# Kernel tuning notes

Measured on AMD Instinct MI355X. Metric: run time of the kernel, lower is better.

The kernel has to match this reference:

```python
import jax, jax.numpy as jnp
import numpy as np
import math

N_HEAD = 16
HEAD_QKV = 1024  # total qkv width; head_dim = HEAD_QKV // N_HEAD
WM_DECAY_LENGTH = 2048
WM_DECAY_RATE = 1.0
WM_ECHOIC = 16


def decay_weight_matrix(n):
    # power_law decay, faithful to get_decay_weight_matrix
    dl = WM_DECAY_LENGTH - WM_ECHOIC + 1
    nums = jnp.linspace(0.0, 1.0, dl)
    decay_values = 1.0 - jnp.power(nums, 1.0 / (np.e * WM_DECAY_RATE))
    decay_values = jnp.concatenate([jnp.ones(WM_ECHOIC - 1), decay_values])  # [WM_DECAY_LENGTH]
    decay_values = decay_values[:n]
    idx = jnp.arange(n)[:, None] - jnp.arange(n)[None, :]  # [n,n], negative above diag
    mat = decay_values[jnp.clip(idx, 0, n - 1)]
    return jnp.tril(mat).astype(jnp.float32)


def setup_inputs() -> dict:
    key = jax.random.key(0)
    k1, k2, k3 = jax.random.split(key, 3)
    B, T, C = 2, 2048, 1024
    x = jax.random.normal(k1, (B, T, C), dtype=jnp.float32)
    W_attn = jax.random.normal(k2, (C, 3 * HEAD_QKV), dtype=jnp.float32) * (1.0 / math.sqrt(C))
    W_proj = jax.random.normal(k3, (HEAD_QKV, C), dtype=jnp.float32) * (1.0 / math.sqrt(HEAD_QKV))
    return {"x": x, "W_attn": W_attn, "W_proj": W_proj}


def reference(x, W_attn, W_proj):
    B, T, C = x.shape
    hd = HEAD_QKV // N_HEAD
    qkv = x @ W_attn  # [B,T,3*HEAD_QKV]
    q, k, v = jnp.split(qkv, 3, axis=-1)
    # [B,T,HQKV] -> [B,H,T,hd]
    q = q.reshape(B, T, N_HEAD, hd).transpose(0, 2, 1, 3)
    k = k.reshape(B, T, N_HEAD, hd).transpose(0, 2, 1, 3)
    v = v.reshape(B, T, N_HEAD, hd).transpose(0, 2, 1, 3)
    att = jnp.einsum('bhqd,bhkd->bhqk', q, k) * (1.0 / math.sqrt(hd))
    causal = jnp.tril(jnp.ones((T, T), dtype=bool))
    att = jnp.where(causal, att, -jnp.inf)
    att = jax.nn.softmax(att, axis=-1)
    att = att * decay_weight_matrix(T)  # post-softmax multiplicative decay
    y = jnp.einsum('bhqk,bhkd->bhqd', att, v)
    y = y.transpose(0, 2, 1, 3).reshape(B, T, HEAD_QKV)
    return y @ W_proj
```

## Files before the change

kernel.cpp:

```cpp
#include <hip/hip_runtime.h>
#include <math.h>

#define B_  2
#define T_  2048
#define C_  1024
#define NH_ 16
#define HD_ 64
#define N3_ 3072

typedef float f32x4 __attribute__((ext_vector_type(4)));
typedef short bf16x8 __attribute__((ext_vector_type(8)));
typedef unsigned short u16;
typedef float f32x4_base __attribute__((ext_vector_type(4)));
typedef f32x4_base __attribute__((aligned(4))) f32x4u;

#define QSCALE 0.18033688011112042f

#if __has_builtin(__builtin_amdgcn_exp2f)
#define EXP2(x) __builtin_amdgcn_exp2f(x)
#else
#define EXP2(x) exp2f(x)
#endif

__device__ __forceinline__ u16 f2bf(float x) {
  unsigned int u = __builtin_bit_cast(unsigned int, x);
  u += 0x7FFFu + ((u >> 16) & 1u);
  return (u16)(u >> 16);
}

__device__ __forceinline__ unsigned int cvt_pk_bf16(float lo, float hi) {
  unsigned int r;
  asm("v_cvt_pk_bf16_f32 %0, %1, %2" : "=v"(r) : "v"(lo), "v"(hi));
  return r;
}

#define GLD16(g, l) __builtin_amdgcn_global_load_lds( \
    (__attribute__((address_space(1))) void*)(g), \
    (__attribute__((address_space(3))) void*)(l), 16, 0, 0)

__global__ __launch_bounds__(256) void prep_kernel(
    const float* __restrict__ x, u16* __restrict__ xb,
    const float* __restrict__ Wa, u16* __restrict__ WaT,
    const float* __restrict__ Wp, u16* __restrict__ WpT,
    float* __restrict__ decR)
{
  __shared__ float tile[32][33];
  const int bid = blockIdx.x;
  const int tid = threadIdx.x;
  if (bid < 4096) {
    int i = (bid * 256 + tid) * 4;
    float4 v = *(const float4*)(x + i);
    ushort4 o;
    o.x = f2bf(v.x); o.y = f2bf(v.y); o.z = f2bf(v.z); o.w = f2bf(v.w);
    *(ushort4*)(xb + i) = o;
  } else if (bid < 8192) {
    const float* in; u16* out; int Cc, c0, r0;
    if (bid < 7168) {
      int t = bid - 4096;
      in = Wa; out = WaT; Cc = N3_;
      c0 = (t % 96) * 32; r0 = (t / 96) * 32;
    } else {
      int t = bid - 7168;
      in = Wp; out = WpT; Cc = C_;
      c0 = (t % 32) * 32; r0 = (t / 32) * 32;
    }
    int tx = tid & 31, ty = tid >> 5;
#pragma unroll
    for (int rr = ty; rr < 32; rr += 8)
      tile[rr][tx] = in[(size_t)(r0 + rr) * Cc + c0 + tx];
    __syncthreads();
#pragma unroll
    for (int rr = ty; rr < 32; rr += 8)
      out[(size_t)(c0 + rr) * 1024 + r0 + tx] = f2bf(tile[tx][rr]);
  } else {
    int j = (bid - 8192) * 256 + tid;
    if (j < 4352) {
      int d = 2047 - j;
      float v = 1.0f;
      if (d >= 15) v = 1.0f - powf((float)(d - 15) * (1.0f / 2032.0f), 0.36787944117144233f);
      decR[j] = v;
    }
  }
}

template<int MODE>
__global__ __launch_bounds__(256, 3) void gemm128_kernel(
    const u16* __restrict__ A, const u16* __restrict__ Bt,
    float* __restrict__ Cf, u16* __restrict__ Cq, u16* __restrict__ Vt,
    int M, int N, int K)
{
  __shared__ char lds[49152];
  const int lane = threadIdx.x & 63;
  const int wave = threadIdx.x >> 6;
  const int nxb = N >> 7;
  const int orig = blockIdx.x;
  const int cpx = (int)gridDim.x >> 3;
  const int wg = (orig & 7) * cpx + (orig >> 3);
  const int m0 = (wg / nxb) << 7;
  const int n0 = (wg % nxb) << 7;
  const int wm = wave >> 1, wn = wave & 1;

  f32x4 acc[4][4] = {};

#define GSTAGE(buf, k0)                                                          \
  {                                                                              \
    _Pragma("unroll")                                                            \
    for (int c = 0; c < 2; ++c) {                                                \
      int chunk = wave * 2048 + c * 1024;                                        \
      int row = (chunk >> 6) + (lane >> 2);                                      \
      int wb = ((lane & 3) << 4) ^ ((row & 3) << 4);                             \
      GLD16((const char*)(A  + (size_t)(m0 + row) * K + (k0)) + wb,              \
            lds + (buf) * 16384 + chunk);                                        \
      GLD16((const char*)(Bt + (size_t)(n0 + row) * K + (k0)) + wb,              \
            lds + (buf) * 16384 + 8192 + chunk);                                 \
    }                                                                            \
  }

  const int nk = K >> 5;
  GSTAGE(0, 0);
  GSTAGE(1, 32);
  __syncthreads();

  for (int i = 0; i < nk; ++i) {
    if (i + 1 < nk) asm volatile("s_waitcnt vmcnt(4)" ::: "memory");
    else            asm volatile("s_waitcnt vmcnt(0)" ::: "memory");
    __builtin_amdgcn_s_barrier();
    __builtin_amdgcn_sched_barrier(0);
    if (i + 2 < nk) GSTAGE((i + 2) % 3, (i + 2) * 32);

    const char* base = lds + (i % 3) * 16384;
    bf16x8 af[4], bfr[4];
#pragma unroll
    for (int m = 0; m < 4; ++m) {
      int row = wm * 64 + m * 16 + (lane & 15);
      int wb = ((lane >> 4) << 4) ^ ((row & 3) << 4);
      af[m] = *(const bf16x8*)(base + row * 64 + wb);
    }
#pragma unroll
    for (int n = 0; n < 4; ++n) {
      int row = wn * 64 + n * 16 + (lane & 15);
      int wb = ((lane >> 4) << 4) ^ ((row & 3) << 4);
      bfr[n] = *(const bf16x8*)(base + 8192 + row * 64 + wb);
    }
    __builtin_amdgcn_s_setprio(1);
#pragma unroll
    for (int m = 0; m < 4; ++m)
#pragma unroll
      for (int n = 0; n < 4; ++n)
        acc[m][n] = __builtin_amdgcn_mfma_f32_16x16x32_bf16(af[m], bfr[n], acc[m][n], 0, 0, 0);
    __builtin_amdgcn_s_setprio(0);
  }

#pragma unroll
  for (int m = 0; m < 4; ++m) {
    int grow0 = m0 + wm * 64 + m * 16 + ((lane >> 4) << 2);
#pragma unroll
    for (int n = 0; n < 4; ++n) {
      int gcol = n0 + wn * 64 + n * 16 + (lane & 15);
      f32x4 v = acc[m][n];
      if (MODE == 0) {
        int bb = grow0 >> 11, tt0 = grow0 & 2047;
        int which = gcol >> 10, rem = gcol & 1023;
        int hh = rem >> 6, dd = rem & 63;
        if (which < 2) {
#pragma unroll
          for (int r = 0; r < 4; ++r) {
            float ov = (which == 0) ? v[r] * QSCALE : v[r];
            Cq[((size_t)(which * 32 + bb * 16 + hh) * 2048 + tt0 + r) * 64 + dd] = f2bf(ov);
          }
        } else {
          ushort4 o;
          o.x = f2bf(v[0]); o.y = f2bf(v[1]); o.z = f2bf(v[2]); o.w = f2bf(v[3]);
          *(ushort4*)(Vt + ((size_t)(bb * 16 + hh) * 64 + dd) * 2048 + tt0) = o;
        }
      } else {
#pragma unroll
        for (int r = 0; r < 4; ++r)
          Cf[(size_t)(grow0 + r) * N + gcol] = v[r];
      }
    }
  }
#undef GSTAGE
}

__global__ __launch_bounds__(256, 2) void attn_kernel(
    const u16* __restrict__ qkb, const u16* __restrict__ vtg,
    const float* __restrict__ decR, u16* __restrict__ yb)
{
  __shared__ char klds[2][8192];
  __shared__ char vlds[2][8192];
  __shared__ u16 plds[128 * 76];

  const int lane = threadIdx.x & 63;
  const int wave = threadIdx.x >> 6;
  const int quad = lane >> 4;
  const int l15 = lane & 15;
  const int orig = blockIdx.x;
  const int xcd = orig & 7;
  const int j = orig >> 3;
  const int bh = xcd * 4 + (j & 3);
  const int tt = j >> 2;
  const int qtA = (tt < 8) ? tt : 23 - tt;
  const int qtB = 31 - qtA;
  const int b = bh >> 4, h = bh & 15;

  const u16* Q   = qkb + (size_t)bh * T_ * HD_;
  const u16* Kg  = qkb + (size_t)(32 + bh) * T_ * HD_;
  const u16* VTg = vtg + (size_t)bh * HD_ * T_;

  const int wrowB = qtB * 64 + wave * 16;
  const int wrowA = qtA * 64 + wave * 16;
  const int qB = wrowB + l15;
  const int qA = wrowA + l15;
  const float* dpB = decR + (2047 - qB + quad * 4);
  const float* dpA = decR + (2047 - qA + quad * 4);

  bf16x8 qaB[2], qaA[2];
  { const u16* qp = Q + (size_t)qB * HD_ + quad * 8;
    qaB[0] = *(const bf16x8*)qp; qaB[1] = *(const bf16x8*)(qp + 32); }
  { const u16* qp = Q + (size_t)qA * HD_ + quad * 8;
    qaA[0] = *(const bf16x8*)qp; qaA[1] = *(const bf16x8*)(qp + 32); }

  f32x4 accB[4] = {}, accA[4] = {};
  float lsumB = 0.0f, lsumA = 0.0f;

#define ASTAGE(buf, kt)                                                          \
  {                                                                              \
    _Pragma("unroll")                                                            \
    for (int c = 0; c < 2; ++c) {                                                \
      int chunk = wave * 2048 + c * 1024;                                        \
      int row = (chunk >> 7) + (lane >> 3);                                      \
      int wb = ((lane & 7) << 4) ^ ((row & 7) << 4);                             \
      GLD16((const char*)(Kg + (size_t)((kt) * 64 + row) * HD_) + wb,            \
            klds[buf] + chunk);                                                  \
      GLD16((const char*)(VTg + (size_t)row * T_ + (kt) * 64) + wb,              \
            vlds[buf] + chunk);                                                  \
    }                                                                            \
  }

  f32x4 dBc[4], dAc[4], dBn[4], dAn[4];
#pragma unroll
  for (int f = 0; f < 4; ++f) {
    dBn[f] = *(const f32x4u*)(dpB + f * 16);
    dAn[f] = *(const f32x4u*)(dpA + f * 16);
  }
  ASTAGE(0, 0);
  __syncthreads();

  const int nkt = qtB + 1;
  for (int kt = 0; kt < nkt; ++kt) {
    const int cur = kt & 1;
#pragma unroll
    for (int f = 0; f < 4; ++f) { dBc[f] = dBn[f]; dAc[f] = dAn[f]; }
    const float* dB1 = dpB + (kt + 1) * 64;
    const float* dA1 = dpA + (kt + 1) * 64;
#pragma unroll
    for (int f = 0; f < 4; ++f) {
      dBn[f] = *(const f32x4u*)(dB1 + f * 16);
      dAn[f] = *(const f32x4u*)(dA1 + f * 16);
    }
    asm volatile("s_waitcnt vmcnt(8)" ::: "memory");
    __builtin_amdgcn_s_barrier();
    __builtin_amdgcn_sched_barrier(0);
    if (kt + 1 < nkt) ASTAGE(cur ^ 1, kt + 1);

    const bool actA = (kt <= qtA);

    bf16x8 kf[4][2];
#pragma unroll
    for (int f = 0; f < 4; ++f) {
      int krow = f * 16 + l15;
      int base = krow * 128;
      int msk = (krow & 7) << 4;
      kf[f][0] = *(const bf16x8*)(klds[cur] + base + ((quad * 16) ^ msk));
      kf[f][1] = *(const bf16x8*)(klds[cur] + base + ((64 + quad * 16) ^ msk));
    }

    f32x4 sB[4], sA[4];
    __builtin_amdgcn_s_setprio(1);
#pragma unroll
    for (int f = 0; f < 4; ++f) {
      f32x4 t = {};
      t = __builtin_amdgcn_mfma_f32_16x16x32_bf16(kf[f][0], qaB[0], t, 0, 0, 0);
      t = __builtin_amdgcn_mfma_f32_16x16x32_bf16(kf[f][1], qaB[1], t, 0, 0, 0);
      sB[f] = t;
    }
    if (actA) {
#pragma unroll
      for (int f = 0; f < 4; ++f) {
        f32x4 t = {};
        t = __builtin_amdgcn_mfma_f32_16x16x32_bf16(kf[f][0], qaA[0], t, 0, 0, 0);
        t = __builtin_amdgcn_mfma_f32_16x16x32_bf16(kf[f][1], qaA[1], t, 0, 0, 0);
        sA[f] = t;
      }
    }
    __builtin_amdgcn_s_setprio(0);

    if (kt == qtB) {
#pragma unroll
      for (int f = 0; f < 4; ++f) {
        int key0 = kt * 64 + f * 16 + quad * 4;
#pragma unroll
        for (int r = 0; r < 4; ++r)
          if (key0 + r > qB) sB[f][r] = -1e30f;
      }
    }
    if (actA && kt == qtA) {
#pragma unroll
      for (int f = 0; f < 4; ++f) {
        int key0 = kt * 64 + f * 16 + quad * 4;
#pragma unroll
        for (int r = 0; r < 4; ++r)
          if (key0 + r > qA) sA[f][r] = -1e30f;
      }
    }

#pragma unroll
    for (int f = 0; f < 4; ++f) {
      f32x4 p;
#pragma unroll
      for (int r = 0; r < 4; ++r) p[r] = EXP2(sB[f][r]);
      lsumB += (p[0] + p[1]) + (p[2] + p[3]);
      unsigned int w0 = cvt_pk_bf16(p[0] * dBc[f][0], p[1] * dBc[f][1]);
      unsigned int w1 = cvt_pk_bf16(p[2] * dBc[f][2], p[3] * dBc[f][3]);
      uint2 wv; wv.x = w0; wv.y = w1;
      *(uint2*)(plds + (size_t)(wave * 16 + l15) * 76 + f * 16 + quad * 4) = wv;
    }
    if (actA) {
#pragma unroll
      for (int f = 0; f < 4; ++f) {
        f32x4 p;
#pragma unroll
        for (int r = 0; r < 4; ++r) p[r] = EXP2(sA[f][r]);
        lsumA += (p[0] + p[1]) + (p[2] + p[3]);
        unsigned int w0 = cvt_pk_bf16(p[0] * dAc[f][0], p[1] * dAc[f][1]);
        unsigned int w1 = cvt_pk_bf16(p[2] * dAc[f][2], p[3] * dAc[f][3]);
        uint2 wv; wv.x = w0; wv.y = w1;
        *(uint2*)(plds + (size_t)(64 + wave * 16 + l15) * 76 + f * 16 + quad * 4) = wv;
      }
    }

    bf16x8 vf[4][2];
#pragma unroll
    for (int n = 0; n < 4; ++n) {
      int vrow = n * 16 + l15;
      int mskv = (vrow & 7) << 4;
#pragma unroll
      for (int ks = 0; ks < 2; ++ks)
        vf[n][ks] = *(const bf16x8*)(vlds[cur] + vrow * 128 + ((ks * 64 + quad * 16) ^ mskv));
    }

    __builtin_amdgcn_s_setprio(1);
#pragma unroll
    for (int ks = 0; ks < 2; ++ks) {
      bf16x8 pa = *(const bf16x8*)(plds + (size_t)(wave * 16 + l15) * 76 + ks * 32 + quad * 8);
#pragma unroll
      for (int n = 0; n < 4; ++n)
        accB[n] = __builtin_amdgcn_mfma_f32_16x16x32_bf16(pa, vf[n][ks], accB[n], 0, 0, 0);
    }
    if (actA) {
#pragma unroll
      for (int ks = 0; ks < 2; ++ks) {
        bf16x8 pa = *(const bf16x8*)(plds + (size_t)(64 + wave * 16 + l15) * 76 + ks * 32 + quad * 8);
#pragma unroll
        for (int n = 0; n < 4; ++n)
          accA[n] = __builtin_amdgcn_mfma_f32_16x16x32_bf16(pa, vf[n][ks], accA[n], 0, 0, 0);
      }
    }
    __builtin_amdgcn_s_setprio(0);
  }
#undef ASTAGE

  lsumB += __shfl_xor(lsumB, 16); lsumB += __shfl_xor(lsumB, 32);
  lsumA += __shfl_xor(lsumA, 16); lsumA += __shfl_xor(lsumA, 32);
  float rB[4], rA[4];
#pragma unroll
  for (int r = 0; r < 4; ++r) {
    rB[r] = 1.0f / __shfl(lsumB, quad * 4 + r, 16);
    rA[r] = 1.0f / __shfl(lsumA, quad * 4 + r, 16);
  }
#pragma unroll
  for (int n = 0; n < 4; ++n) {
    int d = h * 64 + n * 16 + l15;
#pragma unroll
    for (int r = 0; r < 4; ++r) {
      int tB = wrowB + quad * 4 + r;
      int tA = wrowA + quad * 4 + r;
      yb[((size_t)b * T_ + tB) * 1024 + d] = f2bf(accB[n][r] * rB[r]);
      yb[((size_t)b * T_ + tA) * 1024 + d] = f2bf(accA[n][r] * rA[r]);
    }
  }
}

extern "C" void kernel_launch(void* const* d_in, const int* in_sizes, int n_in,
                              void* d_out, int out_size, void* d_ws, size_t ws_size,
                              hipStream_t stream) {
  const float* x  = (const float*)d_in[0];
  const float* Wa = (const float*)d_in[1];
  const float* Wp = (const float*)d_in[2];
  float* out = (float*)d_out;
  char* ws = (char*)d_ws;

  u16*   xb    = (u16*)(ws + 0);
  u16*   WaT   = (u16*)(ws + 8388608);
  u16*   WpT   = (u16*)(ws + 14680064);
  u16*   qkb   = (u16*)(ws + 16777216);
  float* decR  = (float*)(ws + 33554432);
  u16*   VT    = (u16*)(ws + 41943040);
  u16*   yb    = xb;

  prep_kernel<<<8209, 256, 0, stream>>>(x, xb, Wa, WaT, Wp, WpT, decR);
  gemm128_kernel<0><<<768, 256, 0, stream>>>(
      xb, WaT, nullptr, qkb, VT, B_ * T_, N3_, C_);
  attn_kernel<<<512, 256, 0, stream>>>(qkb, VT, decR, yb);
  gemm128_kernel<1><<<256, 256, 0, stream>>>(
      yb, WpT, out, nullptr, nullptr, B_ * T_, 1024, 1024);
}
```

Before: 104.5 us.

## Rewrite attention with 32x32 MFMA tiles and register-resident P via permlane swap

```diff
diff --git a/kernel.cpp b/kernel.cpp
--- a/kernel.cpp
+++ b/kernel.cpp
@@ -9,6 +9,7 @@
 #define N3_ 3072
 
 typedef float f32x4 __attribute__((ext_vector_type(4)));
+typedef float f32x16 __attribute__((ext_vector_type(16)));
 typedef short bf16x8 __attribute__((ext_vector_type(8)));
 typedef unsigned short u16;
 typedef float f32x4_base __attribute__((ext_vector_type(4)));
@@ -189,40 +190,33 @@
 {
   __shared__ char klds[2][8192];
   __shared__ char vlds[2][8192];
-  __shared__ u16 plds[128 * 76];
 
   const int lane = threadIdx.x & 63;
   const int wave = threadIdx.x >> 6;
-  const int quad = lane >> 4;
-  const int l15 = lane & 15;
+  const int i31 = lane & 31;
+  const int hi = lane >> 5;
   const int orig = blockIdx.x;
   const int xcd = orig & 7;
   const int j = orig >> 3;
   const int bh = xcd * 4 + (j & 3);
   const int tt = j >> 2;
-  const int qtA = (tt < 8) ? tt : 23 - tt;
-  const int qtB = 31 - qtA;
+  const int qt = (tt < 8) ? tt : 23 - tt;
   const int b = bh >> 4, h = bh & 15;
 
   const u16* Q   = qkb + (size_t)bh * T_ * HD_;
   const u16* Kg  = qkb + (size_t)(32 + bh) * T_ * HD_;
   const u16* VTg = vtg + (size_t)bh * HD_ * T_;
 
-  const int wrowB = qtB * 64 + wave * 16;
-  const int wrowA = qtA * 64 + wave * 16;
-  const int qB = wrowB + l15;
-  const int qA = wrowA + l15;
-  const float* dpB = decR + (2047 - qB + quad * 4);
-  const float* dpA = decR + (2047 - qA + quad * 4);
-
-  bf16x8 qaB[2], qaA[2];
-  { const u16* qp = Q + (size_t)qB * HD_ + quad * 8;
-    qaB[0] = *(const bf16x8*)qp; qaB[1] = *(const bf16x8*)(qp + 32); }
-  { const u16* qp = Q + (size_t)qA * HD_ + quad * 8;
-    qaA[0] = *(const bf16x8*)qp; qaA[1] = *(const bf16x8*)(qp + 32); }
-
-  f32x4 accB[4] = {}, accA[4] = {};
-  float lsumB = 0.0f, lsumA = 0.0f;
+  const int q = qt * 128 + wave * 32 + i31;
+  const float* dp = decR + (2047 - q) + hi * 4;
+
+  bf16x8 qa[4];
+#pragma unroll
+  for (int s = 0; s < 4; ++s)
+    qa[s] = *(const bf16x8*)(Q + (size_t)q * HD_ + s * 16 + hi * 8);
+
+  f32x16 accy[2] = {};
+  f32x4 lsum4 = {};
 
 #define ASTAGE(buf, kt)                                                          \
   {                                                                              \
@@ -238,156 +232,119 @@
     }                                                                            \
   }
 
-  f32x4 dBc[4], dAc[4], dBn[4], dAn[4];
-#pragma unroll
-  for (int f = 0; f < 4; ++f) {
-    dBn[f] = *(const f32x4u*)(dpB + f * 16);
-    dAn[f] = *(const f32x4u*)(dpA + f * 16);
-  }
+  f32x4 dc[8], dn[8];
+#pragma unroll
+  for (int g8 = 0; g8 < 8; ++g8)
+    dn[g8] = *(const f32x4u*)(dp + (g8 >> 2) * 32 + (g8 & 3) * 8);
   ASTAGE(0, 0);
   __syncthreads();
 
-  const int nkt = qtB + 1;
+  const int nkt = 2 * qt + 2;
   for (int kt = 0; kt < nkt; ++kt) {
     const int cur = kt & 1;
 #pragma unroll
-    for (int f = 0; f < 4; ++f) { dBc[f] = dBn[f]; dAc[f] = dAn[f]; }
-    const float* dB1 = dpB + (kt + 1) * 64;
-    const float* dA1 = dpA + (kt + 1) * 64;
-#pragma unroll
-    for (int f = 0; f < 4; ++f) {
-      dBn[f] = *(const f32x4u*)(dB1 + f * 16);
-      dAn[f] = *(const f32x4u*)(dA1 + f * 16);
-    }
+    for (int g8 = 0; g8 < 8; ++g8) dc[g8] = dn[g8];
+    const float* dnx = dp + (kt + 1) * 64;
+#pragma unroll
+    for (int g8 = 0; g8 < 8; ++g8)
+      dn[g8] = *(const f32x4u*)(dnx + (g8 >> 2) * 32 + (g8 & 3) * 8);
     asm volatile("s_waitcnt vmcnt(8)" ::: "memory");
     __builtin_amdgcn_s_barrier();
     __builtin_amdgcn_sched_barrier(0);
     if (kt + 1 < nkt) ASTAGE(cur ^ 1, kt + 1);
 
-    const bool actA = (kt <= qtA);
-
-    bf16x8 kf[4][2];
-#pragma unroll
-    for (int f = 0; f < 4; ++f) {
-      int krow = f * 16 + l15;
-      int base = krow * 128;
-      int msk = (krow & 7) << 4;
-      kf[f][0] = *(const bf16x8*)(klds[cur] + base + ((quad * 16) ^ msk));
-      kf[f][1] = *(const bf16x8*)(klds[cur] + base + ((64 + quad * 16) ^ msk));
-    }
-
-    f32x4 sB[4], sA[4];
-    __builtin_amdgcn_s_setprio(1);
-#pragma unroll
-    for (int f = 0; f < 4; ++f) {
-      f32x4 t = {};
-      t = __builtin_amdgcn_mfma_f32_16x16x32_bf16(kf[f][0], qaB[0], t, 0, 0, 0);
-      t = __builtin_amdgcn_mfma_f32_16x16x32_bf16(kf[f][1], qaB[1], t, 0, 0, 0);
-      sB[f] = t;
-    }
-    if (actA) {
-#pragma unroll
-      for (int f = 0; f < 4; ++f) {
-        f32x4 t = {};
-        t = __builtin_amdgcn_mfma_f32_16x16x32_bf16(kf[f][0], qaA[0], t, 0, 0, 0);
-        t = __builtin_amdgcn_mfma_f32_16x16x32_bf16(kf[f][1], qaA[1], t, 0, 0, 0);
-        sA[f] = t;
-      }
-    }
-    __builtin_amdgcn_s_setprio(0);
-
-    if (kt == qtB) {
-#pragma unroll
-      for (int f = 0; f < 4; ++f) {
-        int key0 = kt * 64 + f * 16 + quad * 4;
-#pragma unroll
-        for (int r = 0; r < 4; ++r)
-          if (key0 + r > qB) sB[f][r] = -1e30f;
-      }
-    }
-    if (actA && kt == qtA) {
-#pragma unroll
-      for (int f = 0; f < 4; ++f) {
-        int key0 = kt * 64 + f * 16 + quad * 4;
-#pragma unroll
-        for (int r = 0; r < 4; ++r)
-          if (key0 + r > qA) sA[f][r] = -1e30f;
-      }
-    }
-
-#pragma unroll
-    for (int f = 0; f < 4; ++f) {
-      f32x4 p;
-#pragma unroll
-      for (int r = 0; r < 4; ++r) p[r] = EXP2(sB[f][r]);
-      lsumB += (p[0] + p[1]) + (p[2] + p[3]);
-      unsigned int w0 = cvt_pk_bf16(p[0] * dBc[f][0], p[1] * dBc[f][1]);
-      unsigned int w1 = cvt_pk_bf16(p[2] * dBc[f][2], p[3] * dBc[f][3]);
+    const bool active = (kt * 64 <= qt * 128 + wave * 32 + 31);
+    if (active) {
+      f32x16 sacc[2] = {};
+      __builtin_amdgcn_s_setprio(1);
+#pragma unroll
+      for (int kb = 0; kb < 2; ++kb) {
+        int row = kb * 32 + i31;
+        int swz = (row & 7) << 4;
+#pragma unroll
+        for (int s = 0; s < 4; ++s) {
+          bf16x8 kf = *(const bf16x8*)(klds[cur] + row * 128 + ((s * 32 + hi * 16) ^ swz));
+          sacc[kb] = __builtin_amdgcn_mfma_f32_32x32x16_bf16(kf, qa[s], sacc[kb], 0, 0, 0);
+        }
+      }
+      __builtin_amdgcn_s_setprio(0);
+
+      if (kt >= 2 * qt) {
+#pragma unroll
+        for (int kb = 0; kb < 2; ++kb)
+#pragma unroll
+          for (int r = 0; r < 16; ++r) {
+            int key = kt * 64 + kb * 32 + (r & 3) + 8 * (r >> 2) + 4 * hi;
+            sacc[kb][r] = (key > q) ? -1e30f : sacc[kb][r];
+          }
+      }
+
+      unsigned int uu[2][4][2];
+#pragma unroll
+      for (int kb = 0; kb < 2; ++kb)
+#pragma unroll
+        for (int g = 0; g < 4; ++g) {
+          f32x4 p;
+#pragma unroll
+          for (int e = 0; e < 4; ++e) p[e] = EXP2(sacc[kb][g * 4 + e]);
+          lsum4 += p;
+          f32x4 d4 = dc[kb * 4 + g];
+          uu[kb][g][0] = cvt_pk_bf16(p[0] * d4[0], p[1] * d4[1]);
+          uu[kb][g][1] = cvt_pk_bf16(p[2] * d4[2], p[3] * d4[3]);
+        }
+
+      bf16x8 pb[4];
+#pragma unroll
+      for (int s = 0; s < 4; ++s) {
+        int kb = s >> 1, gg = (s & 1) * 2;
+        unsigned int a  = uu[kb][gg][0],     b2 = uu[kb][gg][1];
+        unsigned int c  = uu[kb][gg + 1][0], d2 = uu[kb][gg + 1][1];
+        asm volatile("v_permlane32_swap_b32 %0, %1" : "+v"(a),  "+v"(c));
+        asm volatile("v_permlane32_swap_b32 %0, %1" : "+v"(b2), "+v"(d2));
+        int4 w; w.x = (int)a; w.y = (int)b2; w.z = (int)c; w.w = (int)d2;
+        pb[s] = __builtin_bit_cast(bf16x8, w);
+      }
+
+      __builtin_amdgcn_s_setprio(1);
+#pragma unroll
+      for (int db = 0; db < 2; ++db) {
+        int row = db * 32 + i31;
+        int swz = (row & 7) << 4;
+#pragma unroll
+        for (int s = 0; s < 4; ++s) {
+          bf16x8 vf = *(const bf16x8*)(vlds[cur] + row * 128 + ((s * 32 + hi * 16) ^ swz));
+          accy[db] = __builtin_amdgcn_mfma_f32_32x32x16_bf16(vf, pb[s], accy[db], 0, 0, 0);
+        }
+      }
+      __builtin_amdgcn_s_setprio(0);
+    }
+  }
+#undef ASTAGE
+
+  float lsum = (lsum4[0] + lsum4[1]) + (lsum4[2] + lsum4[3]);
+  lsum += __shfl_xor(lsum, 32);
+  const float rq = 1.0f / lsum;
+
+  __syncthreads();
+  char* yt = (char*)klds + wave * 4096;
+#pragma unroll
+  for (int db = 0; db < 2; ++db)
+#pragma unroll
+    for (int g = 0; g < 4; ++g) {
+      unsigned int w0 = cvt_pk_bf16(accy[db][g * 4 + 0] * rq, accy[db][g * 4 + 1] * rq);
+      unsigned int w1 = cvt_pk_bf16(accy[db][g * 4 + 2] * rq, accy[db][g * 4 + 3] * rq);
       uint2 wv; wv.x = w0; wv.y = w1;
-      *(uint2*)(plds + (size_t)(wave * 16 + l15) * 76 + f * 16 + quad * 4) = wv;
-    }
-    if (actA) {
-#pragma unroll
-      for (int f = 0; f < 4; ++f) {
-        f32x4 p;
-#pragma unroll
-        for (int r = 0; r < 4; ++r) p[r] = EXP2(sA[f][r]);
-        lsumA += (p[0] + p[1]) + (p[2] + p[3]);
-        unsigned int w0 = cvt_pk_bf16(p[0] * dAc[f][0], p[1] * dAc[f][1]);
-        unsigned int w1 = cvt_pk_bf16(p[2] * dAc[f][2], p[3] * dAc[f][3]);
-        uint2 wv; wv.x = w0; wv.y = w1;
-        *(uint2*)(plds + (size_t)(64 + wave * 16 + l15) * 76 + f * 16 + quad * 4) = wv;
-      }
-    }
-
-    bf16x8 vf[4][2];
-#pragma unroll
-    for (int n = 0; n < 4; ++n) {
-      int vrow = n * 16 + l15;
-      int mskv = (vrow & 7) << 4;
-#pragma unroll
-      for (int ks = 0; ks < 2; ++ks)
-        vf[n][ks] = *(const bf16x8*)(vlds[cur] + vrow * 128 + ((ks * 64 + quad * 16) ^ mskv));
-    }
-
-    __builtin_amdgcn_s_setprio(1);
-#pragma unroll
-    for (int ks = 0; ks < 2; ++ks) {
-      bf16x8 pa = *(const bf16x8*)(plds + (size_t)(wave * 16 + l15) * 76 + ks * 32 + quad * 8);
-#pragma unroll
-      for (int n = 0; n < 4; ++n)
-        accB[n] = __builtin_amdgcn_mfma_f32_16x16x32_bf16(pa, vf[n][ks], accB[n], 0, 0, 0);
-    }
-    if (actA) {
-#pragma unroll
-      for (int ks = 0; ks < 2; ++ks) {
-        bf16x8 pa = *(const bf16x8*)(plds + (size_t)(64 + wave * 16 + l15) * 76 + ks * 32 + quad * 8);
-#pragma unroll
-        for (int n = 0; n < 4; ++n)
-          accA[n] = __builtin_amdgcn_mfma_f32_16x16x32_bf16(pa, vf[n][ks], accA[n], 0, 0, 0);
-      }
-    }
-    __builtin_amdgcn_s_setprio(0);
-  }
-#undef ASTAGE
-
-  lsumB += __shfl_xor(lsumB, 16); lsumB += __shfl_xor(lsumB, 32);
-  lsumA += __shfl_xor(lsumA, 16); lsumA += __shfl_xor(lsumA, 32);
-  float rB[4], rA[4];
-#pragma unroll
-  for (int r = 0; r < 4; ++r) {
-    rB[r] = 1.0f / __shfl(lsumB, quad * 4 + r, 16);
-    rA[r] = 1.0f / __shfl(lsumA, quad * 4 + r, 16);
-  }
-#pragma unroll
-  for (int n = 0; n < 4; ++n) {
-    int d = h * 64 + n * 16 + l15;
-#pragma unroll
-    for (int r = 0; r < 4; ++r) {
-      int tB = wrowB + quad * 4 + r;
-      int tA = wrowA + quad * 4 + r;
-      yb[((size_t)b * T_ + tB) * 1024 + d] = f2bf(accB[n][r] * rB[r]);
-      yb[((size_t)b * T_ + tA) * 1024 + d] = f2bf(accA[n][r] * rA[r]);
+      *(uint2*)(yt + i31 * 128 + ((db * 64 + g * 16 + hi * 8) ^ ((i31 & 7) << 4))) = wv;
+    }
+  {
+    int qloc = lane >> 1, dh = lane & 1;
+    int tg = qt * 128 + wave * 32 + qloc;
+    u16* dst = yb + ((size_t)b * T_ + tg) * 1024 + h * 64 + dh * 32;
+#pragma unroll
+    for (int c = 0; c < 4; ++c) {
+      int colb = (dh * 64 + c * 16) ^ ((qloc & 7) << 4);
+      int4 vv = *(const int4*)(yt + qloc * 128 + colb);
+      *(int4*)(dst + c * 8) = vv;
     }
   }
 }
```

Result: slower. 107.5 us (+2.9%).

## Serialize paired query tiles into a uniform 33-step loop per block

Applied to the files above, without the earlier changes.

```diff
diff --git a/kernel.cpp b/kernel.cpp
--- a/kernel.cpp
+++ b/kernel.cpp
@@ -189,7 +189,7 @@
 {
   __shared__ char klds[2][8192];
   __shared__ char vlds[2][8192];
-  __shared__ u16 plds[128 * 76];
+  __shared__ u16 plds[64 * 76];
 
   const int lane = threadIdx.x & 63;
   const int wave = threadIdx.x >> 6;
@@ -197,11 +197,10 @@
   const int l15 = lane & 15;
   const int orig = blockIdx.x;
   const int xcd = orig & 7;
-  const int j = orig >> 3;
-  const int bh = xcd * 4 + (j & 3);
-  const int tt = j >> 2;
-  const int qtA = (tt < 8) ? tt : 23 - tt;
-  const int qtB = 31 - qtA;
+  const int bh = xcd * 4 + ((orig >> 3) & 3);
+  const int x = orig >> 5;
+  const int qtA = x;
+  const int qtB = 31 - x;
   const int b = bh >> 4, h = bh & 15;
 
   const u16* Q   = qkb + (size_t)bh * T_ * HD_;
@@ -238,33 +237,34 @@
     }                                                                            \
   }
 
-  f32x4 dBc[4], dAc[4], dBn[4], dAn[4];
-#pragma unroll
-  for (int f = 0; f < 4; ++f) {
-    dBn[f] = *(const f32x4u*)(dpB + f * 16);
-    dAn[f] = *(const f32x4u*)(dpA + f * 16);
-  }
+  const int twoA1 = 2 * qtA + 1;
+
+  f32x4 dc[4], dn[4];
+#pragma unroll
+  for (int f = 0; f < 4; ++f) dn[f] = *(const f32x4u*)(dpB + f * 16);
   ASTAGE(0, 0);
   __syncthreads();
 
-  const int nkt = qtB + 1;
-  for (int kt = 0; kt < nkt; ++kt) {
-    const int cur = kt & 1;
-#pragma unroll
-    for (int f = 0; f < 4; ++f) { dBc[f] = dBn[f]; dAc[f] = dAn[f]; }
-    const float* dB1 = dpB + (kt + 1) * 64;
-    const float* dA1 = dpA + (kt + 1) * 64;
-#pragma unroll
-    for (int f = 0; f < 4; ++f) {
-      dBn[f] = *(const f32x4u*)(dB1 + f * 16);
-      dAn[f] = *(const f32x4u*)(dA1 + f * 16);
-    }
+  for (int u = 0; u < 33; ++u) {
+    const int kt   = (u <= twoA1) ? (u >> 1) : (u - qtA - 1);
+    const int selA = (u <= twoA1) ? (u & 1) : 0;
+    const int cur  = kt & 1;
+
+#pragma unroll
+    for (int f = 0; f < 4; ++f) dc[f] = dn[f];
+    {
+      const int u1 = u + 1;
+      const int kt1   = (u1 <= twoA1) ? (u1 >> 1) : (u1 - qtA - 1);
+      const int selA1 = (u1 <= twoA1) ? (u1 & 1) : 0;
+      const float* dnp = (selA1 ? dpA : dpB) + kt1 * 64;
+#pragma unroll
+      for (int f = 0; f < 4; ++f) dn[f] = *(const f32x4u*)(dnp + f * 16);
+    }
+
     asm volatile("s_waitcnt vmcnt(8)" ::: "memory");
     __builtin_amdgcn_s_barrier();
     __builtin_amdgcn_sched_barrier(0);
-    if (kt + 1 < nkt) ASTAGE(cur ^ 1, kt + 1);
-
-    const bool actA = (kt <= qtA);
+    if (!selA && kt < qtB) ASTAGE(cur ^ 1, kt + 1);
 
     bf16x8 kf[4][2];
 #pragma unroll
@@ -276,69 +276,44 @@
       kf[f][1] = *(const bf16x8*)(klds[cur] + base + ((64 + quad * 16) ^ msk));
     }
 
-    f32x4 sB[4], sA[4];
+    const bf16x8 q0 = selA ? qaA[0] : qaB[0];
+    const bf16x8 q1 = selA ? qaA[1] : qaB[1];
+    f32x4 s[4];
     __builtin_amdgcn_s_setprio(1);
 #pragma unroll
     for (int f = 0; f < 4; ++f) {
       f32x4 t = {};
-      t = __builtin_amdgcn_mfma_f32_16x16x32_bf16(kf[f][0], qaB[0], t, 0, 0, 0);
-      t = __builtin_amdgcn_mfma_f32_16x16x32_bf16(kf[f][1], qaB[1], t, 0, 0, 0);
-      sB[f] = t;
-    }
-    if (actA) {
-#pragma unroll
-      for (int f = 0; f < 4; ++f) {
-        f32x4 t = {};
-        t = __builtin_amdgcn_mfma_f32_16x16x32_bf16(kf[f][0], qaA[0], t, 0, 0, 0);
-        t = __builtin_amdgcn_mfma_f32_16x16x32_bf16(kf[f][1], qaA[1], t, 0, 0, 0);
-        sA[f] = t;
-      }
+      t = __builtin_amdgcn_mfma_f32_16x16x32_bf16(kf[f][0], q0, t, 0, 0, 0);
+      t = __builtin_amdgcn_mfma_f32_16x16x32_bf16(kf[f][1], q1, t, 0, 0, 0);
+      s[f] = t;
     }
     __builtin_amdgcn_s_setprio(0);
 
-    if (kt == qtB) {
+    const int qtsel = selA ? qtA : qtB;
+    if (kt == qtsel) {
+      const int qsel = selA ? qA : qB;
 #pragma unroll
       for (int f = 0; f < 4; ++f) {
         int key0 = kt * 64 + f * 16 + quad * 4;
 #pragma unroll
         for (int r = 0; r < 4; ++r)
-          if (key0 + r > qB) sB[f][r] = -1e30f;
+          if (key0 + r > qsel) s[f][r] = -1e30f;
       }
     }
-    if (actA && kt == qtA) {
-#pragma unroll
-      for (int f = 0; f < 4; ++f) {
-        int key0 = kt * 64 + f * 16 + quad * 4;
-#pragma unroll
-        for (int r = 0; r < 4; ++r)
-          if (key0 + r > qA) sA[f][r] = -1e30f;
-      }
-    }
-
+
+    float ls = 0.0f;
 #pragma unroll
     for (int f = 0; f < 4; ++f) {
       f32x4 p;
 #pragma unroll
-      for (int r = 0; r < 4; ++r) p[r] = EXP2(sB[f][r]);
-      lsumB += (p[0] + p[1]) + (p[2] + p[3]);
-      unsigned int w0 = cvt_pk_bf16(p[0] * dBc[f][0], p[1] * dBc[f][1]);
-      unsigned int w1 = cvt_pk_bf16(p[2] * dBc[f][2], p[3] * dBc[f][3]);
+      for (int r = 0; r < 4; ++r) p[r] = EXP2(s[f][r]);
+      ls += (p[0] + p[1]) + (p[2] + p[3]);
+      unsigned int w0 = cvt_pk_bf16(p[0] * dc[f][0], p[1] * dc[f][1]);
+      unsigned int w1 = cvt_pk_bf16(p[2] * dc[f][2], p[3] * dc[f][3]);
       uint2 wv; wv.x = w0; wv.y = w1;
       *(uint2*)(plds + (size_t)(wave * 16 + l15) * 76 + f * 16 + quad * 4) = wv;
     }
-    if (actA) {
-#pragma unroll
-      for (int f = 0; f < 4; ++f) {
-        f32x4 p;
-#pragma unroll
-        for (int r = 0; r < 4; ++r) p[r] = EXP2(sA[f][r]);
-        lsumA += (p[0] + p[1]) + (p[2] + p[3]);
-        unsigned int w0 = cvt_pk_bf16(p[0] * dAc[f][0], p[1] * dAc[f][1]);
-        unsigned int w1 = cvt_pk_bf16(p[2] * dAc[f][2], p[3] * dAc[f][3]);
-        uint2 wv; wv.x = w0; wv.y = w1;
-        *(uint2*)(plds + (size_t)(64 + wave * 16 + l15) * 76 + f * 16 + quad * 4) = wv;
-      }
-    }
+    if (selA) lsumA += ls; else lsumB += ls;
 
     bf16x8 vf[4][2];
 #pragma unroll
@@ -350,21 +325,20 @@
         vf[n][ks] = *(const bf16x8*)(vlds[cur] + vrow * 128 + ((ks * 64 + quad * 16) ^ mskv));
     }
 
+    bf16x8 pa0 = *(const bf16x8*)(plds + (size_t)(wave * 16 + l15) * 76 + quad * 8);
+    bf16x8 pa1 = *(const bf16x8*)(plds + (size_t)(wave * 16 + l15) * 76 + 32 + quad * 8);
     __builtin_amdgcn_s_setprio(1);
-#pragma unroll
-    for (int ks = 0; ks < 2; ++ks) {
-      bf16x8 pa = *(const bf16x8*)(plds + (size_t)(wave * 16 + l15) * 76 + ks * 32 + quad * 8);
-#pragma unroll
-      for (int n = 0; n < 4; ++n)
-        accB[n] = __builtin_amdgcn_mfma_f32_16x16x32_bf16(pa, vf[n][ks], accB[n], 0, 0, 0);
-    }
-    if (actA) {
-#pragma unroll
-      for (int ks = 0; ks < 2; ++ks) {
-        bf16x8 pa = *(const bf16x8*)(plds + (size_t)(64 + wave * 16 + l15) * 76 + ks * 32 + quad * 8);
-#pragma unroll
-        for (int n = 0; n < 4; ++n)
-          accA[n] = __builtin_amdgcn_mfma_f32_16x16x32_bf16(pa, vf[n][ks], accA[n], 0, 0, 0);
+    if (selA) {
+#pragma unroll
+      for (int n = 0; n < 4; ++n) {
+        accA[n] = __builtin_amdgcn_mfma_f32_16x16x32_bf16(pa0, vf[n][0], accA[n], 0, 0, 0);
+        accA[n] = __builtin_amdgcn_mfma_f32_16x16x32_bf16(pa1, vf[n][1], accA[n], 0, 0, 0);
+      }
+    } else {
+#pragma unroll
+      for (int n = 0; n < 4; ++n) {
+        accB[n] = __builtin_amdgcn_mfma_f32_16x16x32_bf16(pa0, vf[n][0], accB[n], 0, 0, 0);
+        accB[n] = __builtin_amdgcn_mfma_f32_16x16x32_bf16(pa1, vf[n][1], accB[n], 0, 0, 0);
       }
     }
     __builtin_amdgcn_s_setprio(0);
```

Result: no change. 103.8 us (-0.6%).
